# Optimization experiments

Measured on AMD Instinct MI355X. Metric: run time of the kernel, lower is better.

The kernel has to match this reference:

```python
import jax, jax.numpy as jnp
import numpy as np

B, T, C = 4, 2048, 1024
HEAD = 64  # n_embd // n_heads


def setup_inputs() -> dict:
    key = jax.random.key(0)
    kx, kk, kq, kv = jax.random.split(key, 4)
    x = jax.random.normal(kx, (B, T, C), dtype=jnp.float32)
    # nn.Linear(n_embd, head_size, bias=False) weights have shape [head_size, n_embd]
    s = 1.0 / np.sqrt(C)
    Wk = jax.random.normal(kk, (HEAD, C), dtype=jnp.float32) * s
    Wq = jax.random.normal(kq, (HEAD, C), dtype=jnp.float32) * s
    Wv = jax.random.normal(kv, (HEAD, C), dtype=jnp.float32) * s
    return {"x": x, "Wk": Wk, "Wq": Wq, "Wv": Wv}


def reference(x, Wk, Wq, Wv):
    Bx, Tx, Cx = x.shape
    k = jnp.einsum("btc,hc->bth", x, Wk)  # [B,T,HEAD]
    q = jnp.einsum("btc,hc->bth", x, Wq)
    v = jnp.einsum("btc,hc->bth", x, Wv)
    # NOTE: original scales by C**-0.5 (C = n_embd), not head_size**-0.5
    scale = Cx ** (-0.5)
    wei = jnp.einsum("bth,bsh->bts", q, k) * scale  # [B,T,T]
    causal = jnp.tril(jnp.ones((Tx, Tx), dtype=bool))
    wei = jnp.where(causal, wei, -jnp.inf)
    wei = jax.nn.softmax(wei, axis=-1)
    # dropout p=0.0 (eval) -> identity
    out = jnp.einsum("bts,bsh->bth", wei, v)  # [B,T,HEAD]
    return out
```

## Files before the change

### kernel.cpp

```cpp
#include <hip/hip_runtime.h>
#include <math.h>

#define Tn 2048
#define Cn 1024
#define Hn 64

using u16 = unsigned short;
typedef float f32x4 __attribute__((ext_vector_type(4)));
typedef __bf16 bf16x8 __attribute__((ext_vector_type(8)));
typedef u16 u16x8 __attribute__((ext_vector_type(8)));
typedef u16 u16x4 __attribute__((ext_vector_type(4)));

__device__ __forceinline__ u16 f2bf(float f) {
    return __builtin_bit_cast(u16, static_cast<__bf16>(f));
}

__global__ __launch_bounds__(256) void wpack_kernel(
    const float* __restrict__ Wk, const float* __restrict__ Wq,
    const float* __restrict__ Wv, u16* __restrict__ wp)
{
    int slot = blockIdx.x * 256 + threadIdx.x;
    int n16  = slot >> 11;
    int rem  = slot & 2047;
    int kc   = rem >> 6;
    int lane = rem & 63;
    int l15 = lane & 15, lg = lane >> 4;
    int col = n16 * 16 + l15;
    const float* __restrict__ Wm = (col < 64) ? Wk : (col < 128) ? Wq : Wv;
    float sc = (col >= 64 && col < 128) ? 0.03125f : 1.0f;
    const float* src = &Wm[(size_t)(col & 63) * Cn + kc * 32 + lg * 8];
    float4 lo = *reinterpret_cast<const float4*>(src);
    float4 hi = *reinterpret_cast<const float4*>(src + 4);
    u16x8 o;
    o[0] = f2bf(lo.x * sc); o[1] = f2bf(lo.y * sc);
    o[2] = f2bf(lo.z * sc); o[3] = f2bf(lo.w * sc);
    o[4] = f2bf(hi.x * sc); o[5] = f2bf(hi.y * sc);
    o[6] = f2bf(hi.z * sc); o[7] = f2bf(hi.w * sc);
    *reinterpret_cast<u16x8*>(&wp[(size_t)slot * 8]) = o;
}

__global__ __launch_bounds__(512) void qkv_proj(
    const float* __restrict__ x, const u16* __restrict__ wp,
    u16* __restrict__ kb, u16* __restrict__ qb, u16* __restrict__ vb)
{
    __shared__ float xs[2][32 * 68];

    const int tid  = threadIdx.x;
    const int lane = tid & 63;
    const int w    = tid >> 6;
    const int rg   = w & 1;
    const int cg   = w >> 1;
    const int l15  = lane & 15;
    const int lg   = lane >> 4;

    const int row0 = blockIdx.x * 32;
    const int sr   = tid >> 4;
    const int scc  = (tid & 15) << 2;

    f32x4 acc[3];
#pragma unroll
    for (int nt = 0; nt < 3; ++nt)
#pragma unroll
        for (int r = 0; r < 4; ++r) acc[nt][r] = 0.f;

    const float* __restrict__ xsrc = &x[(size_t)(row0 + sr) * Cn + scc];

    float4 g = *reinterpret_cast<const float4*>(xsrc);
    *reinterpret_cast<float4*>(&xs[0][sr * 68 + scc]) = g;
    __syncthreads();

    for (int ks = 0; ks < 16; ++ks) {
        const int cur = ks & 1;
        if (ks < 15)
            g = *reinterpret_cast<const float4*>(xsrc + (ks + 1) * 64);
#pragma unroll
        for (int kc2 = 0; kc2 < 2; ++kc2) {
            const float* ap = &xs[cur][(rg * 16 + l15) * 68 + kc2 * 32 + (lg << 3)];
            f32x4 a0 = *reinterpret_cast<const f32x4*>(ap);
            f32x4 a1 = *reinterpret_cast<const f32x4*>(ap + 4);
            bf16x8 a;
            a[0] = (__bf16)a0[0]; a[1] = (__bf16)a0[1];
            a[2] = (__bf16)a0[2]; a[3] = (__bf16)a0[3];
            a[4] = (__bf16)a1[0]; a[5] = (__bf16)a1[1];
            a[6] = (__bf16)a1[2]; a[7] = (__bf16)a1[3];
            const int kcg = ks * 2 + kc2;
#pragma unroll
            for (int nt = 0; nt < 3; ++nt) {
                const int n16 = cg * 3 + nt;
                bf16x8 bfr = *reinterpret_cast<const bf16x8*>(
                    &wp[(size_t)((n16 * 32 + kcg) * 64 + lane) * 8]);
                acc[nt] = __builtin_amdgcn_mfma_f32_16x16x32_bf16(a, bfr, acc[nt], 0, 0, 0);
            }
        }
        if (ks < 15)
            *reinterpret_cast<float4*>(&xs[cur ^ 1][sr * 68 + scc]) = g;
        __syncthreads();
    }

#pragma unroll
    for (int nt = 0; nt < 3; ++nt) {
        const int n16  = cg * 3 + nt;
        const int col0 = n16 * 16;
        const int mat  = col0 >> 6;
        u16* __restrict__ ob = (mat == 0) ? kb : (mat == 1) ? qb : vb;
        const int h = (col0 & 63) + l15;
#pragma unroll
        for (int reg = 0; reg < 4; ++reg) {
            const int grow = row0 + rg * 16 + (lg << 2) + reg;
            ob[(size_t)grow * Hn + h] = f2bf(acc[nt][reg]);
        }
    }
}

__global__ __launch_bounds__(256) void attn(
    const u16* __restrict__ qb, const u16* __restrict__ kb,
    const u16* __restrict__ vb, float* __restrict__ Opart,
    float* __restrict__ mlb)
{
    __shared__ u16 Ks[2][64 * 72];
    __shared__ u16 VTs[2][64 * 72];
    __shared__ u16 Pl[4][16 * 72];

    const int tid  = threadIdx.x;
    const int lane = tid & 63;
    const int w    = tid >> 6;
    const int g    = w >> 1;
    const int p    = w & 1;
    const int l15  = lane & 15;
    const int lg   = lane >> 4;

    const int bid = blockIdx.x;
    const int b = bid / 288;
    const int r = bid % 288;
    int gq = (int)((sqrtf((float)r + 1.0f) - 1.0f) * 0.5f);
    while (4 * (gq + 1) * (gq + 2) <= r) ++gq;
    while (4 * gq * (gq + 1) > r) --gq;
    const int rr = r - 4 * gq * (gq + 1);
    const int qt = gq * 8 + rr / (gq + 1);
    const int c  = rr % (gq + 1);

    const int t0  = qt * 32;
    const int wr0 = t0 + g * 16;
    const int nkt = ((t0 + 31) >> 6) + 1;
    const size_t kvbase = (size_t)b * Tn * Hn;

    bf16x8 qf[2];
    {
        const u16* qrow = qb + ((size_t)(b * Tn + wr0 + l15)) * Hn;
        qf[0] = *reinterpret_cast<const bf16x8*>(&qrow[(lg << 3)]);
        qf[1] = *reinterpret_cast<const bf16x8*>(&qrow[32 + (lg << 3)]);
    }

    f32x4 o[4];
    float m[4], ls[4];
#pragma unroll
    for (int nt = 0; nt < 4; ++nt)
#pragma unroll
        for (int rg2 = 0; rg2 < 4; ++rg2) o[nt][rg2] = 0.f;
#pragma unroll
    for (int rg2 = 0; rg2 < 4; ++rg2) { m[rg2] = -INFINITY; ls[rg2] = 0.f; }

    for (int s = 0; s < 2; ++s) {
        const int kt0 = c * 4 + 2 * s, kt1 = kt0 + 1;
        if (kt0 < nkt) {
#pragma unroll
            for (int i = 0; i < 2; ++i) {
                int cc = tid + 256 * i;
                int rr2 = cc >> 3, c8 = (cc & 7) << 3;
                *reinterpret_cast<u16x8*>(&Ks[0][rr2 * 72 + c8]) =
                    *reinterpret_cast<const u16x8*>(&kb[kvbase + (size_t)(kt0 * 64 + rr2) * Hn + c8]);
            }
#pragma unroll
            for (int i = 0; i < 2; ++i) {
                int cc = tid + 256 * i;
                int k = cc & 63, d0 = (cc >> 6) << 3;
                u16x8 v = *reinterpret_cast<const u16x8*>(&vb[kvbase + (size_t)(kt0 * 64 + k) * Hn + d0]);
#pragma unroll
                for (int j = 0; j < 8; ++j) VTs[0][(d0 + j) * 72 + k] = v[j];
            }
        }
        if (kt1 < nkt) {
#pragma unroll
            for (int i = 0; i < 2; ++i) {
                int cc = tid + 256 * i;
                int rr2 = cc >> 3, c8 = (cc & 7) << 3;
                *reinterpret_cast<u16x8*>(&Ks[1][rr2 * 72 + c8]) =
                    *reinterpret_cast<const u16x8*>(&kb[kvbase + (size_t)(kt1 * 64 + rr2) * Hn + c8]);
            }
#pragma unroll
            for (int i = 0; i < 2; ++i) {
                int cc = tid + 256 * i;
                int k = cc & 63, d0 = (cc >> 6) << 3;
                u16x8 v = *reinterpret_cast<const u16x8*>(&vb[kvbase + (size_t)(kt1 * 64 + k) * Hn + d0]);
#pragma unroll
                for (int j = 0; j < 8; ++j) VTs[1][(d0 + j) * 72 + k] = v[j];
            }
        }
        __syncthreads();

        const int mykt = kt0 + p;
        if (mykt < nkt) {
            f32x4 sf[4];
#pragma unroll
            for (int nt = 0; nt < 4; ++nt)
#pragma unroll
                for (int rg2 = 0; rg2 < 4; ++rg2) sf[nt][rg2] = 0.f;
#pragma unroll
            for (int kc = 0; kc < 2; ++kc) {
#pragma unroll
                for (int nt = 0; nt < 4; ++nt) {
                    bf16x8 kf = *reinterpret_cast<const bf16x8*>(
                        &Ks[p][(nt * 16 + l15) * 72 + kc * 32 + (lg << 3)]);
                    sf[nt] = __builtin_amdgcn_mfma_f32_16x16x32_bf16(qf[kc], kf, sf[nt], 0, 0, 0);
                }
            }
            if (mykt * 64 + 63 > wr0) {
#pragma unroll
                for (int nt = 0; nt < 4; ++nt) {
                    int kg = mykt * 64 + nt * 16 + l15;
#pragma unroll
                    for (int reg = 0; reg < 4; ++reg) {
                        int tq = wr0 + (lg << 2) + reg;
                        if (kg > tq) sf[nt][reg] = -INFINITY;
                    }
                }
            }
            float pv[4][4];
#pragma unroll
            for (int reg = 0; reg < 4; ++reg) {
                float tm = fmaxf(fmaxf(sf[0][reg], sf[1][reg]),
                                 fmaxf(sf[2][reg], sf[3][reg]));
#pragma unroll
                for (int off = 1; off < 16; off <<= 1)
                    tm = fmaxf(tm, __shfl_xor(tm, off, 64));
                float nm = fmaxf(m[reg], tm);
                float al = __expf(m[reg] - nm);
                float rs = 0.f;
#pragma unroll
                for (int nt = 0; nt < 4; ++nt) {
                    pv[nt][reg] = __expf(sf[nt][reg] - nm);
                    rs += pv[nt][reg];
                }
#pragma unroll
                for (int off = 1; off < 16; off <<= 1)
                    rs += __shfl_xor(rs, off, 64);
                ls[reg] = ls[reg] * al + rs;
                m[reg]  = nm;
#pragma unroll
                for (int nt = 0; nt < 4; ++nt) o[nt][reg] *= al;
            }
#pragma unroll
            for (int nt = 0; nt < 4; ++nt)
#pragma unroll
                for (int reg = 0; reg < 4; ++reg)
                    Pl[w][((lg << 2) + reg) * 72 + nt * 16 + l15] = f2bf(pv[nt][reg]);
#pragma unroll
            for (int kc = 0; kc < 2; ++kc) {
                bf16x8 pa = *reinterpret_cast<const bf16x8*>(
                    &Pl[w][l15 * 72 + kc * 32 + (lg << 3)]);
#pragma unroll
                for (int nt = 0; nt < 4; ++nt) {
                    bf16x8 vf = *reinterpret_cast<const bf16x8*>(
                        &VTs[p][(nt * 16 + l15) * 72 + kc * 32 + (lg << 3)]);
                    o[nt] = __builtin_amdgcn_mfma_f32_16x16x32_bf16(pa, vf, o[nt], 0, 0, 0);
                }
            }
        }
        __syncthreads();
    }

    float* slab = reinterpret_cast<float*>(&Ks[0][0]);
    float* sb = slab + g * (24 * 64);
    if (p == 1) {
#pragma unroll
        for (int nt = 0; nt < 4; ++nt)
#pragma unroll
            for (int reg = 0; reg < 4; ++reg)
                sb[(nt * 4 + reg) * 64 + lane] = o[nt][reg];
#pragma unroll
        for (int reg = 0; reg < 4; ++reg) {
            sb[(16 + reg) * 64 + lane] = m[reg];
            sb[(20 + reg) * 64 + lane] = ls[reg];
        }
    }
    __syncthreads();
    if (p == 0) {
        const size_t pidx = (size_t)(b * 64 + qt) * 8 + c;
        float* __restrict__ ob = Opart + pidx * 2048;
#pragma unroll
        for (int reg = 0; reg < 4; ++reg) {
            float mB = sb[(16 + reg) * 64 + lane];
            float lB = sb[(20 + reg) * 64 + lane];
            float ms = fmaxf(m[reg], mB);
            float aA = __expf(m[reg] - ms);
            float aB = __expf(mB - ms);
            int row32 = g * 16 + (lg << 2) + reg;
            if (l15 == 0) {
                float* mlp = mlb + pidx * 64 + row32 * 2;
                mlp[0] = ms;
                mlp[1] = aA * ls[reg] + aB * lB;
            }
#pragma unroll
            for (int nt = 0; nt < 4; ++nt)
                ob[row32 * 64 + nt * 16 + l15] =
                    aA * o[nt][reg] + aB * sb[(nt * 4 + reg) * 64 + lane];
        }
    }
}

__global__ __launch_bounds__(256) void attn_merge(
    const float* __restrict__ Opart, const float* __restrict__ mlb,
    float* __restrict__ out)
{
    const int bid = blockIdx.x;
    const int b = bid >> 6, qt = bid & 63;
    const int nch = (qt >> 3) + 1;
    const int t = threadIdx.x;
    const int row = t >> 3, d0 = (t & 7) << 3;
    const size_t pbase = (size_t)(b * 64 + qt) * 8;

    float m = -INFINITY, l = 0.f;
    f32x4 O0 = {0.f, 0.f, 0.f, 0.f}, O1 = {0.f, 0.f, 0.f, 0.f};
    for (int cc = 0; cc < nch; ++cc) {
        const float* mlp = mlb + (pbase + cc) * 64 + row * 2;
        float mc = mlp[0], lc = mlp[1];
        float nm = fmaxf(m, mc);
        float a  = __expf(m - nm);
        float ac = __expf(mc - nm);
        const float* op = Opart + (pbase + cc) * 2048 + row * 64 + d0;
        f32x4 c0 = *reinterpret_cast<const f32x4*>(op);
        f32x4 c1 = *reinterpret_cast<const f32x4*>(op + 4);
        O0 = O0 * a + c0 * ac;
        O1 = O1 * a + c1 * ac;
        l  = l * a + lc * ac;
        m  = nm;
    }
    float inv = 1.f / l;
    float* orow = out + ((size_t)(b * Tn + qt * 32 + row)) * Hn + d0;
    *reinterpret_cast<f32x4*>(orow)     = O0 * inv;
    *reinterpret_cast<f32x4*>(orow + 4) = O1 * inv;
}

extern "C" void kernel_launch(void* const* d_in, const int* in_sizes, int n_in,
                              void* d_out, int out_size, void* d_ws, size_t ws_size,
                              hipStream_t stream) {
    const float* x  = (const float*)d_in[0];
    const float* Wk = (const float*)d_in[1];
    const float* Wq = (const float*)d_in[2];
    const float* Wv = (const float*)d_in[3];
    float* out = (float*)d_out;

    const size_t rows = (size_t)4 * Tn;
    u16* kbuf = (u16*)d_ws;
    u16* qbuf = kbuf + rows * Hn;
    u16* vbuf = qbuf + rows * Hn;
    u16* wpk  = vbuf + rows * Hn;
    float* Opart = (float*)(wpk + 196608);
    float* mlb   = Opart + (size_t)4 * 64 * 8 * 2048;

    wpack_kernel<<<96, 256, 0, stream>>>(Wk, Wq, Wv, wpk);
    qkv_proj<<<256, 512, 0, stream>>>(x, wpk, kbuf, qbuf, vbuf);
    attn<<<1152, 256, 0, stream>>>(qbuf, kbuf, vbuf, Opart, mlb);
    attn_merge<<<256, 256, 0, stream>>>(Opart, mlb, out);
}
```

Before: 47.21 us.

## Load all KV tiles upfront via direct-to-LDS with swizzle, lazy rescale, parallel merge

The attention kernel now loads all four K/V tiles of a chunk at once, one wave per tile. K goes through global_load_lds into an XOR-swizzled unpadded layout and V is transposed into swizzled LDS, which removes the per-step barriers and padded layouts. It adds setprio around the MFMA blocks and a lazy softmax rescale that skips the running-max update when the new max stays within a threshold. The merge kernel loads all partial stats first, computes the final max once, and then accumulates the partial outputs without serial exp chains. The cost is doubled LDS footprint, which can lower occupancy, and the lazy rescale relies on bounded score growth.

After: 52.55 us. +11.3%, slower.

```diff
diff --git a/kernel.cpp b/kernel.cpp
--- a/kernel.cpp
+++ b/kernel.cpp
@@ -14,6 +14,11 @@
 __device__ __forceinline__ u16 f2bf(float f) {
     return __builtin_bit_cast(u16, static_cast<__bf16>(f));
 }
+
+#define SWI(r, c) ((r) * 64 + ((c) ^ (((r) & 7) << 3)))
+
+#define LDS3(p) ((__attribute__((address_space(3))) void*)(p))
+#define GLB1(p) ((const __attribute__((address_space(1))) void*)(p))
 
 __global__ __launch_bounds__(256) void wpack_kernel(
     const float* __restrict__ Wk, const float* __restrict__ Wq,
@@ -117,8 +122,8 @@
     const u16* __restrict__ vb, float* __restrict__ Opart,
     float* __restrict__ mlb)
 {
-    __shared__ u16 Ks[2][64 * 72];
-    __shared__ u16 VTs[2][64 * 72];
+    __shared__ u16 Ks[4][64 * 64];
+    __shared__ u16 VTs[4][64 * 64];
     __shared__ u16 Pl[4][16 * 72];
 
     const int tid  = threadIdx.x;
@@ -138,10 +143,12 @@
     const int rr = r - 4 * gq * (gq + 1);
     const int qt = gq * 8 + rr / (gq + 1);
     const int c  = rr % (gq + 1);
+    const int c4 = c * 4;
 
     const int t0  = qt * 32;
     const int wr0 = t0 + g * 16;
     const int nkt = ((t0 + 31) >> 6) + 1;
+    int ntt = nkt - c4; if (ntt > 4) ntt = 4;
     const size_t kvbase = (size_t)b * Tn * Hn;
 
     bf16x8 qf[2];
@@ -151,6 +158,29 @@
         qf[1] = *reinterpret_cast<const bf16x8*>(&qrow[32 + (lg << 3)]);
     }
 
+    if (w < ntt) {
+        const int kt = c4 + w;
+        const u16* __restrict__ ksrc = kb + kvbase + (size_t)kt * 64 * Hn;
+        const u16* __restrict__ vsrc = vb + kvbase + (size_t)(kt * 64 + lane) * Hn;
+#pragma unroll
+        for (int i = 0; i < 8; ++i) {
+            const int rw = i * 8 + (lane >> 3);
+            const int co = (((lane & 7) ^ (rw & 7)) << 3);
+            __builtin_amdgcn_global_load_lds(
+                GLB1(ksrc + rw * Hn + co), LDS3(&Ks[w][i * 512]), 16, 0, 0);
+        }
+        u16x8 vr[8];
+#pragma unroll
+        for (int i = 0; i < 8; ++i)
+            vr[i] = *reinterpret_cast<const u16x8*>(&vsrc[i * 8]);
+#pragma unroll
+        for (int i = 0; i < 8; ++i)
+#pragma unroll
+            for (int j = 0; j < 8; ++j)
+                VTs[w][SWI(i * 8 + j, lane)] = vr[i][j];
+    }
+    __syncthreads();
+
     f32x4 o[4];
     float m[4], ls[4];
 #pragma unroll
@@ -160,60 +190,27 @@
 #pragma unroll
     for (int rg2 = 0; rg2 < 4; ++rg2) { m[rg2] = -INFINITY; ls[rg2] = 0.f; }
 
+#pragma unroll
     for (int s = 0; s < 2; ++s) {
-        const int kt0 = c * 4 + 2 * s, kt1 = kt0 + 1;
-        if (kt0 < nkt) {
-#pragma unroll
-            for (int i = 0; i < 2; ++i) {
-                int cc = tid + 256 * i;
-                int rr2 = cc >> 3, c8 = (cc & 7) << 3;
-                *reinterpret_cast<u16x8*>(&Ks[0][rr2 * 72 + c8]) =
-                    *reinterpret_cast<const u16x8*>(&kb[kvbase + (size_t)(kt0 * 64 + rr2) * Hn + c8]);
-            }
-#pragma unroll
-            for (int i = 0; i < 2; ++i) {
-                int cc = tid + 256 * i;
-                int k = cc & 63, d0 = (cc >> 6) << 3;
-                u16x8 v = *reinterpret_cast<const u16x8*>(&vb[kvbase + (size_t)(kt0 * 64 + k) * Hn + d0]);
-#pragma unroll
-                for (int j = 0; j < 8; ++j) VTs[0][(d0 + j) * 72 + k] = v[j];
-            }
-        }
-        if (kt1 < nkt) {
-#pragma unroll
-            for (int i = 0; i < 2; ++i) {
-                int cc = tid + 256 * i;
-                int rr2 = cc >> 3, c8 = (cc & 7) << 3;
-                *reinterpret_cast<u16x8*>(&Ks[1][rr2 * 72 + c8]) =
-                    *reinterpret_cast<const u16x8*>(&kb[kvbase + (size_t)(kt1 * 64 + rr2) * Hn + c8]);
-            }
-#pragma unroll
-            for (int i = 0; i < 2; ++i) {
-                int cc = tid + 256 * i;
-                int k = cc & 63, d0 = (cc >> 6) << 3;
-                u16x8 v = *reinterpret_cast<const u16x8*>(&vb[kvbase + (size_t)(kt1 * 64 + k) * Hn + d0]);
-#pragma unroll
-                for (int j = 0; j < 8; ++j) VTs[1][(d0 + j) * 72 + k] = v[j];
-            }
-        }
-        __syncthreads();
-
-        const int mykt = kt0 + p;
+        const int tt = 2 * s + p;
+        const int mykt = c4 + tt;
         if (mykt < nkt) {
             f32x4 sf[4];
 #pragma unroll
             for (int nt = 0; nt < 4; ++nt)
 #pragma unroll
                 for (int rg2 = 0; rg2 < 4; ++rg2) sf[nt][rg2] = 0.f;
+            __builtin_amdgcn_s_setprio(1);
 #pragma unroll
             for (int kc = 0; kc < 2; ++kc) {
 #pragma unroll
                 for (int nt = 0; nt < 4; ++nt) {
                     bf16x8 kf = *reinterpret_cast<const bf16x8*>(
-                        &Ks[p][(nt * 16 + l15) * 72 + kc * 32 + (lg << 3)]);
+                        &Ks[tt][SWI(nt * 16 + l15, kc * 32 + (lg << 3))]);
                     sf[nt] = __builtin_amdgcn_mfma_f32_16x16x32_bf16(qf[kc], kf, sf[nt], 0, 0, 0);
                 }
             }
+            __builtin_amdgcn_s_setprio(0);
             if (mykt * 64 + 63 > wr0) {
 #pragma unroll
                 for (int nt = 0; nt < 4; ++nt) {
@@ -225,29 +222,42 @@
                     }
                 }
             }
+            float tm[4];
+            bool defok = true;
+#pragma unroll
+            for (int reg = 0; reg < 4; ++reg) {
+                float t = fmaxf(fmaxf(sf[0][reg], sf[1][reg]),
+                                fmaxf(sf[2][reg], sf[3][reg]));
+#pragma unroll
+                for (int off = 1; off < 16; off <<= 1)
+                    t = fmaxf(t, __shfl_xor(t, off, 64));
+                tm[reg] = t;
+                defok = defok && (t <= m[reg] + 8.f);
+            }
+            if (!__all(defok ? 1 : 0)) {
+#pragma unroll
+                for (int reg = 0; reg < 4; ++reg) {
+                    float nm = fmaxf(m[reg], tm[reg]);
+                    float al = __expf(m[reg] - nm);
+                    ls[reg] *= al;
+#pragma unroll
+                    for (int nt = 0; nt < 4; ++nt) o[nt][reg] *= al;
+                    m[reg] = nm;
+                }
+            }
             float pv[4][4];
 #pragma unroll
             for (int reg = 0; reg < 4; ++reg) {
-                float tm = fmaxf(fmaxf(sf[0][reg], sf[1][reg]),
-                                 fmaxf(sf[2][reg], sf[3][reg]));
-#pragma unroll
-                for (int off = 1; off < 16; off <<= 1)
-                    tm = fmaxf(tm, __shfl_xor(tm, off, 64));
-                float nm = fmaxf(m[reg], tm);
-                float al = __expf(m[reg] - nm);
                 float rs = 0.f;
 #pragma unroll
                 for (int nt = 0; nt < 4; ++nt) {
-                    pv[nt][reg] = __expf(sf[nt][reg] - nm);
+                    pv[nt][reg] = __expf(sf[nt][reg] - m[reg]);
                     rs += pv[nt][reg];
                 }
 #pragma unroll
                 for (int off = 1; off < 16; off <<= 1)
                     rs += __shfl_xor(rs, off, 64);
-                ls[reg] = ls[reg] * al + rs;
-                m[reg]  = nm;
-#pragma unroll
-                for (int nt = 0; nt < 4; ++nt) o[nt][reg] *= al;
+                ls[reg] += rs;
             }
 #pragma unroll
             for (int nt = 0; nt < 4; ++nt)
@@ -258,17 +268,19 @@
             for (int kc = 0; kc < 2; ++kc) {
                 bf16x8 pa = *reinterpret_cast<const bf16x8*>(
                     &Pl[w][l15 * 72 + kc * 32 + (lg << 3)]);
+                __builtin_amdgcn_s_setprio(1);
 #pragma unroll
                 for (int nt = 0; nt < 4; ++nt) {
                     bf16x8 vf = *reinterpret_cast<const bf16x8*>(
-                        &VTs[p][(nt * 16 + l15) * 72 + kc * 32 + (lg << 3)]);
+                        &VTs[tt][SWI(nt * 16 + l15, kc * 32 + (lg << 3))]);
                     o[nt] = __builtin_amdgcn_mfma_f32_16x16x32_bf16(pa, vf, o[nt], 0, 0, 0);
                 }
-            }
-        }
-        __syncthreads();
-    }
-
+                __builtin_amdgcn_s_setprio(0);
+            }
+        }
+    }
+
+    __syncthreads();
     float* slab = reinterpret_cast<float*>(&Ks[0][0]);
     float* sb = slab + g * (24 * 64);
     if (p == 1) {
@@ -319,21 +331,36 @@
     const int row = t >> 3, d0 = (t & 7) << 3;
     const size_t pbase = (size_t)(b * 64 + qt) * 8;
 
-    float m = -INFINITY, l = 0.f;
+    float mc[8], lc[8];
+#pragma unroll
+    for (int cc = 0; cc < 8; ++cc) {
+        if (cc < nch) {
+            const float* mlp = mlb + (pbase + cc) * 64 + row * 2;
+            mc[cc] = mlp[0];
+            lc[cc] = mlp[1];
+        } else { mc[cc] = -INFINITY; lc[cc] = 0.f; }
+    }
+    float mfin = mc[0];
+#pragma unroll
+    for (int cc = 1; cc < 8; ++cc) mfin = fmaxf(mfin, mc[cc]);
+
+    float wgt[8], l = 0.f;
+#pragma unroll
+    for (int cc = 0; cc < 8; ++cc) {
+        wgt[cc] = (cc < nch) ? __expf(mc[cc] - mfin) : 0.f;
+        l += lc[cc] * wgt[cc];
+    }
+
     f32x4 O0 = {0.f, 0.f, 0.f, 0.f}, O1 = {0.f, 0.f, 0.f, 0.f};
-    for (int cc = 0; cc < nch; ++cc) {
-        const float* mlp = mlb + (pbase + cc) * 64 + row * 2;
-        float mc = mlp[0], lc = mlp[1];
-        float nm = fmaxf(m, mc);
-        float a  = __expf(m - nm);
-        float ac = __expf(mc - nm);
-        const float* op = Opart + (pbase + cc) * 2048 + row * 64 + d0;
-        f32x4 c0 = *reinterpret_cast<const f32x4*>(op);
-        f32x4 c1 = *reinterpret_cast<const f32x4*>(op + 4);
-        O0 = O0 * a + c0 * ac;
-        O1 = O1 * a + c1 * ac;
-        l  = l * a + lc * ac;
-        m  = nm;
+#pragma unroll
+    for (int cc = 0; cc < 8; ++cc) {
+        if (cc < nch) {
+            const float* op = Opart + (pbase + cc) * 2048 + row * 64 + d0;
+            f32x4 c0 = *reinterpret_cast<const f32x4*>(op);
+            f32x4 c1 = *reinterpret_cast<const f32x4*>(op + 4);
+            O0 += c0 * wgt[cc];
+            O1 += c1 * wgt[cc];
+        }
     }
     float inv = 1.f / l;
     float* orow = out + ((size_t)(b * Tn + qt * 32 + row)) * Hn + d0;
```
